# Performance work log

Hardware: AMD Instinct MI355X
Metric: run time of the kernel (lower is better)

## Reference

```python
import jax, jax.numpy as jnp
import numpy as np

B, C, H, W = 4, 64, 128, 128
HID = 256
Q = H * W


def setup_inputs() -> dict:
    key = jax.random.key(0)
    ks = jax.random.split(key, 8)
    inp = jax.random.normal(ks[0], (B, C, H, W), jnp.float32)
    coord = jax.random.uniform(ks[1], (B, Q, 2), jnp.float32, -1.0, 1.0)
    # cell ~ 2/H (size of a high-res pixel in normalized coords), slightly jittered
    cell = (2.0 / H) * (1.0 + 0.1 * jax.random.uniform(ks[2], (B, Q, 2), jnp.float32))
    sc = 1.0 / np.sqrt(C * 9)
    coef_w = jax.random.normal(ks[3], (HID, C, 3, 3), jnp.float32) * sc
    coef_b = jax.random.normal(ks[4], (HID,), jnp.float32) * 0.01
    freq_w = jax.random.normal(ks[5], (HID, C, 3, 3), jnp.float32) * sc
    freq_b = jax.random.normal(ks[6], (HID,), jnp.float32) * 0.01
    phase_w = jax.random.normal(ks[7], (HID // 2, 2), jnp.float32) * 0.5
    return dict(inp=inp, coord=coord, cell=cell, coef_w=coef_w, coef_b=coef_b,
                freq_w=freq_w, freq_b=freq_b, phase_w=phase_w)


def _conv3(x, w, b):
    # 3x3 conv, stride 1, pad 1, NCHW
    y = jax.lax.conv_general_dilated(x, w, (1, 1), ((1, 1), (1, 1)),
                                     dimension_numbers=('NCHW', 'OIHW', 'NCHW'))
    return y + b[None, :, None, None]


def reference(inp, coord, cell, coef_w, coef_b, freq_w, freq_b, phase_w):
    bs, q = coord.shape[0], coord.shape[1]
    h, w = inp.shape[2], inp.shape[3]
    coef = _conv3(inp, coef_w, coef_b)           # (B,HID,H,W)
    freq = _conv3(inp, freq_w, freq_b)           # (B,HID,H,W)
    coef_f = coef.reshape(bs, -1, h * w)
    freq_f = freq.reshape(bs, -1, h * w)
    rx = 1.0 / h                                 # 2/h/2
    ry = 1.0 / w
    eps_shift = 1e-6
    hw = jnp.array([h, w], jnp.float32)
    rel_cell = cell * hw                         # (B,Q,2)
    phase = rel_cell @ phase_w.T                 # (B,Q,HID//2)
    outputs, areas = [], []
    last_raw_area = None
    for vx in (-1.0, 1.0):
        for vy in (-1.0, 1.0):
            c = coord + jnp.array([vx * rx + eps_shift, vy * ry + eps_shift], jnp.float32)
            c = jnp.clip(c, -1.0 + 1e-6, 1.0 - 1e-6)
            # nearest grid_sample, align_corners=False (round-half-even like nearbyint)
            iy = jnp.round(((c[..., 0] + 1.0) * h - 1.0) * 0.5)
            ix = jnp.round(((c[..., 1] + 1.0) * w - 1.0) * 0.5)
            iy = jax.lax.stop_gradient(jnp.clip(iy, 0, h - 1).astype(jnp.int32))
            ix = jax.lax.stop_gradient(jnp.clip(ix, 0, w - 1).astype(jnp.int32))
            idx = iy * w + ix                    # (B,Q)
            q_coef = jnp.take_along_axis(coef_f, idx[:, None, :], axis=2).transpose(0, 2, 1)  # (B,Q,HID)
            q_freq = jnp.take_along_axis(freq_f, idx[:, None, :], axis=2).transpose(0, 2, 1)
            # make_coord value at the gathered pixel
            q_coord = jnp.stack([-1.0 + (2.0 * iy.astype(jnp.float32) + 1.0) / h,
                                 -1.0 + (2.0 * ix.astype(jnp.float32) + 1.0) / w], axis=-1)
            rel = (coord - q_coord) * hw         # (B,Q,2)
            # split q_freq into consecutive pairs, stack -> (B,Q,2,HID//2)
            f = q_freq.reshape(bs, q, -1, 2).swapaxes(-1, -2)
            f = jnp.sum(f * rel[..., None], axis=-2) + phase     # (B,Q,HID//2)
            f = jnp.concatenate([jnp.cos(jnp.pi * f), jnp.sin(jnp.pi * f)], axis=-1)  # (B,Q,HID)
            out = (q_coef * f).reshape(bs, h, w, -1).transpose(0, 3, 1, 2)  # (B,HID,H,W)
            last_raw_area = jnp.abs(rel[..., 0] * rel[..., 1])
            outputs.append(out)
            areas.append(last_raw_area + 1e-9)
    tot_area = areas[0] + areas[1] + areas[2] + areas[3]
    # Faithful to the source: a SINGLE weight from the last corner's raw area
    # is applied to every corner output (the per-corner area swap is unused).
    weight = (last_raw_area / tot_area).reshape(bs, h, w, 1).transpose(0, 3, 1, 2)
    ret = (outputs[0] + outputs[1] + outputs[2] + outputs[3]) * weight
    return ret
```

## Files before the change

kernel.cpp:

```cpp
#include <hip/hip_runtime.h>

typedef unsigned short u16;
typedef _Float16 f16;

#define CIN   64
#define HH    128
#define WW    128
#define NPIX  16384
#define HID   256
#define MTOT  512
#define KTOT  576
#define NB    4
#define WELEM 294912
#define XROW  130
#define XROWS 16900

#define SHM  ((float)(-0.0078125 + 1e-6))
#define SHP  ((float)( 0.0078125 + 1e-6))
#define CLO  ((float)(-1.0 + 1e-6))
#define CHI  ((float)( 1.0 - 1e-6))
#define PIF  3.14159265358979323846f

#define QSCL  1024.0f
#define QISCL (1.0f / 1024.0f)

using f32x4 = __attribute__((ext_vector_type(4))) float;
using f16x8 = __attribute__((ext_vector_type(8))) _Float16;

typedef __attribute__((address_space(1))) const void gas_void;
typedef __attribute__((address_space(3))) void las_void;
__device__ __forceinline__ void gload16(const void* g, void* l) {
  __builtin_amdgcn_global_load_lds((gas_void*)g, (las_void*)l, 16, 0, 0);
}

__device__ __forceinline__ float ldq(const short* p) { return (float)(*p) * QISCL; }
__device__ __forceinline__ void ldqpair(const short* p, float& a, float& b) {
  int u = *(const int*)p;
  a = (float)((short)(u & 0xFFFF)) * QISCL;
  b = (float)((short)(u >> 16)) * QISCL;
}
__device__ __forceinline__ unsigned packq(float a, float b) {
  float fa = fminf(fmaxf(a * QSCL, -32767.f), 32767.f);
  float fb = fminf(fmaxf(b * QSCL, -32767.f), 32767.f);
  int ia = (int)rintf(fa), ib = (int)rintf(fb);
  return ((unsigned)(unsigned short)(short)ia) | (((unsigned)(unsigned short)(short)ib) << 16);
}
__device__ __forceinline__ void storeq4(short* p, float a, float b, float c, float d) {
  uint2 v; v.x = packq(a, b); v.y = packq(c, d);
  *(uint2*)p = v;
}

__global__ __launch_bounds__(256) void lte_prep_w(
    const float* __restrict__ cw, const float* __restrict__ fw,
    f16* __restrict__ Awp) {
  int id = blockIdx.x * 256 + threadIdx.x;
  if (id >= WELEM) return;
  int e  = id & 7;
  int j  = (id >> 3) & 7;
  int i  = (id >> 6) & 127;
  int t2 = id >> 13;
  int mt = t2 / 9;
  int s  = t2 - mt * 9;
  int ch = ((j ^ (i & 7)) << 3) + e;
  int m  = mt * 128 + i;
  const float* src = (m < HID) ? cw : fw;
  Awp[id] = (f16)src[(m & 255) * KTOT + ch * 9 + s];
}

__global__ __launch_bounds__(256) void lte_prep_x(
    const float* __restrict__ inp, f16* __restrict__ xp) {
  int id = blockIdx.x * 256 + threadIdx.x;
  if (id >= NB * XROWS) return;
  int b  = id / XROWS;
  int rr = id - b * XROWS;
  int yy = rr / XROW;
  int x  = rr - yy * XROW - 1;
  int y  = yy - 1;
  f16* op = xp + (size_t)id * 64;
  if ((unsigned)y < 128u && (unsigned)x < 128u) {
    const float* ip = inp + (size_t)b * CIN * NPIX + y * WW + x;
#pragma unroll
    for (int q = 0; q < 8; ++q) {
      f16x8 v;
#pragma unroll
      for (int k = 0; k < 8; ++k) v[k] = (f16)ip[(q * 8 + k) * NPIX];
      *(f16x8*)(op + q * 8) = v;
    }
  } else {
    f16x8 z = {};
#pragma unroll
    for (int q = 0; q < 8; ++q) *(f16x8*)(op + q * 8) = z;
  }
}

__global__ __launch_bounds__(256) void lte_conv_gemm(
    const f16* __restrict__ xp, const f16* __restrict__ Awp,
    const float* __restrict__ coef_b, const float* __restrict__ freq_b,
    short* __restrict__ YT) {
  __shared__ f16 As[2][128 * 64];
  __shared__ f16 Bs[2][128 * 64];

  const int t  = threadIdx.x;
  const int bx = blockIdx.x;
  const int mt = blockIdx.y;
  const int bb = blockIdx.z;
  const int l  = t & 63;
  const int w  = t >> 6;
  const int wr = w >> 1, wc = w & 1;
  const int lm = l & 15;
  const int lm7 = lm & 7;
  const int kq = l >> 4;
  const int lrow = l >> 3;
  const int lchk = l & 7;
  const int w8 = w * 8;

  f32x4 acc[4][4] = {};

  const f16* Atile = Awp + (size_t)(mt * 9) * 8192;
  const f16* xb = xp + (size_t)bb * XROWS * 64;

  auto stage = [&](int s, f16* Ad, f16* Bd) {
    const int ky = s / 3, kx = s - 3 * (s / 3);
    const f16* asrc = Atile + s * 8192;
    const int grow0 = (bx + ky) * XROW + kx;
#pragma unroll
    for (int i = 0; i < 8; ++i) {
      const int c = w8 + i;
      if (c < 16) {
        gload16(asrc + c * 512 + l * 8, Ad + c * 512);
      } else {
        const int cb = c - 16;
        gload16(xb + (size_t)(grow0 + cb * 8 + lrow) * 64 + ((lchk ^ lrow) << 3),
                Bd + cb * 512);
      }
    }
  };

  stage(0, As[0], Bs[0]);
  asm volatile("s_waitcnt vmcnt(0)" ::: "memory");
  __builtin_amdgcn_s_barrier();
  __builtin_amdgcn_sched_barrier(0);

  for (int s = 0; s < 9; ++s) {
    const int cur = s & 1;
    if (s < 8) stage(s + 1, As[cur ^ 1], Bs[cur ^ 1]);
    const f16* Ac = As[cur];
    const f16* Bc = Bs[cur];
#pragma unroll
    for (int ks = 0; ks < 2; ++ks) {
      const int jl = ks * 4 + kq;
      const int pc = (jl ^ lm7) << 3;
      f16x8 af[4], bg[4];
#pragma unroll
      for (int mi = 0; mi < 4; ++mi)
        af[mi] = *(const f16x8*)&Ac[(wr * 64 + mi * 16 + lm) * 64 + pc];
#pragma unroll
      for (int ni = 0; ni < 4; ++ni)
        bg[ni] = *(const f16x8*)&Bc[(wc * 64 + ni * 16 + lm) * 64 + pc];
#pragma unroll
      for (int mi = 0; mi < 4; ++mi)
#pragma unroll
        for (int ni = 0; ni < 4; ++ni)
          acc[mi][ni] = __builtin_amdgcn_mfma_f32_16x16x32_f16(af[mi], bg[ni], acc[mi][ni], 0, 0, 0);
    }
    if (s < 8) {
      asm volatile("s_waitcnt vmcnt(0)" ::: "memory");
      __builtin_amdgcn_s_barrier();
      __builtin_amdgcn_sched_barrier(0);
    }
  }

  const float* bias = (mt < 2) ? (coef_b + mt * 128) : (freq_b + (mt - 2) * 128);
  const int rj = (l >> 4) * 4;
#pragma unroll
  for (int mi = 0; mi < 4; ++mi) {
    const int bm = wr * 64 + mi * 16 + rj;
    const float b0 = bias[bm], b1 = bias[bm + 1], b2 = bias[bm + 2], b3 = bias[bm + 3];
#pragma unroll
    for (int ni = 0; ni < 4; ++ni) {
      const int p = bx * 128 + wc * 64 + ni * 16 + lm;
      size_t off = ((size_t)(bb * NPIX + p)) * 512 + mt * 128 + bm;
      f32x4 v = acc[mi][ni];
      storeq4(&YT[off], v[0] + b0, v[1] + b1, v[2] + b2, v[3] + b3);
    }
  }
}

__global__ __launch_bounds__(128) void lte_sample(
    const short* __restrict__ YT, const float* __restrict__ coord,
    const float* __restrict__ cell, const float* __restrict__ phase_w,
    float* __restrict__ out) {
  __shared__ float lout[256 * 17];
  const int j     = threadIdx.x;
  const int q0    = blockIdx.x * 16;
  const int b     = q0 >> 14;
  const int q0loc = q0 & (NPIX - 1);
  const float pw0 = phase_w[2 * j], pw1 = phase_w[2 * j + 1];
  const short* Yb = YT + ((size_t)b * NPIX) * 512;

  for (int qi = 0; qi < 16; ++qi) {
    const int qg = q0 + qi;
    const float c0  = coord[2 * qg], c1 = coord[2 * qg + 1];
    const float ce0 = cell[2 * qg],  ce1 = cell[2 * qg + 1];
    const float ph  = (ce0 * 128.0f) * pw0 + (ce1 * 128.0f) * pw1;
    float accC = 0.f, accS = 0.f, tot = 0.f, a3 = 0.f;
#pragma unroll
    for (int ci = 0; ci < 4; ++ci) {
      const float s0 = (ci & 2) ? SHP : SHM;
      const float s1 = (ci & 1) ? SHP : SHM;
      float cx = fminf(fmaxf(c0 + s0, CLO), CHI);
      float cy = fminf(fmaxf(c1 + s1, CLO), CHI);
      float ty = ((cx + 1.0f) * 128.0f - 1.0f) * 0.5f;
      float tx = ((cy + 1.0f) * 128.0f - 1.0f) * 0.5f;
      float fy = fminf(fmaxf(rintf(ty), 0.f), 127.f);
      float fx = fminf(fmaxf(rintf(tx), 0.f), 127.f);
      int iy = (int)fy, ix = (int)fx;
      float qcy = -1.0f + (2.0f * fy + 1.0f) * (1.0f / 128.0f);
      float qcx = -1.0f + (2.0f * fx + 1.0f) * (1.0f / 128.0f);
      float rel0 = (c0 - qcy) * 128.0f;
      float rel1 = (c1 - qcx) * 128.0f;
      float ar = fabsf(rel0 * rel1);
      tot += ar + 1e-9f;
      if (ci == 3) a3 = ar;
      const short* bp = Yb + ((size_t)(iy * 128 + ix)) * 512;
      float coefA = ldq(bp + j);
      float coefB = ldq(bp + 128 + j);
      float f0, f1;
      ldqpair(bp + 256 + 2 * j, f0, f1);
      float f = f0 * rel0 + f1 * rel1 + ph;
      float ang = PIF * f;
      accC += coefA * __cosf(ang);
      accS += coefB * __sinf(ang);
    }
    const float wgt = a3 / tot;
    lout[j * 17 + qi]         = accC * wgt;
    lout[(j + 128) * 17 + qi] = accS * wgt;
  }
  __syncthreads();
#pragma unroll
  for (int pass = 0; pass < 8; ++pass) {
    int c  = pass * 32 + (j >> 2);
    int qf = (j & 3) * 4;
    float4 v;
    v.x = lout[c * 17 + qf];     v.y = lout[c * 17 + qf + 1];
    v.z = lout[c * 17 + qf + 2]; v.w = lout[c * 17 + qf + 3];
    *(float4*)(out + (((size_t)(b * 256 + c)) << 14) + q0loc + qf) = v;
  }
}

extern "C" void kernel_launch(void* const* d_in, const int* in_sizes, int n_in,
                              void* d_out, int out_size, void* d_ws, size_t ws_size,
                              hipStream_t stream) {
  const float* inp     = (const float*)d_in[0];
  const float* coord   = (const float*)d_in[1];
  const float* cell    = (const float*)d_in[2];
  const float* coef_w  = (const float*)d_in[3];
  const float* coef_b  = (const float*)d_in[4];
  const float* freq_w  = (const float*)d_in[5];
  const float* freq_b  = (const float*)d_in[6];
  const float* phase_w = (const float*)d_in[7];
  float* out = (float*)d_out;

  f16* Awp = (f16*)d_ws;
  f16* xp  = (f16*)((char*)d_ws + (size_t)WELEM * 2);
  short* YT = (short*)((char*)d_ws + (size_t)WELEM * 2 + (size_t)NB * XROWS * 64 * 2);

  lte_prep_w<<<dim3(1152), dim3(256), 0, stream>>>(coef_w, freq_w, Awp);
  lte_prep_x<<<dim3((NB * XROWS + 255) / 256), dim3(256), 0, stream>>>(inp, xp);
  lte_conv_gemm<<<dim3(128, 4, 4), dim3(256), 0, stream>>>(xp, Awp, coef_b, freq_b, YT);
  lte_sample<<<dim3(4096), dim3(128), 0, stream>>>(YT, coord, cell, phase_w, out);
}
```

Baseline: 126.1 us.

## Load input halo once per conv block and enlarge GEMM tile to 256x256

The conv GEMM block now covers 256 output channels by two image rows (256 pixels) with 512 threads. It loads a 4x136-pixel halo of the padded input into shared memory once, instead of reloading shifted input tiles for each of the nine 3x3 taps. Only the weight tiles stay double-buffered per tap. The input prep kernel now pre-swizzles channel chunks per column so the shifted shared-memory reads stay conflict-free. The trade-off is a larger shared-memory footprint, more accumulators per thread and fewer blocks. The workspace offset also grows, presumably to cover halo reads past the end of the input.

Measured after the change: 129.9 us. 1.03x slower.

```diff
diff --git a/kernel.cpp b/kernel.cpp
--- a/kernel.cpp
+++ b/kernel.cpp
@@ -57,14 +57,13 @@
   if (id >= WELEM) return;
   int e  = id & 7;
   int j  = (id >> 3) & 7;
-  int i  = (id >> 6) & 127;
-  int t2 = id >> 13;
+  int i  = (id >> 6) & 255;
+  int t2 = id >> 14;
   int mt = t2 / 9;
   int s  = t2 - mt * 9;
   int ch = ((j ^ (i & 7)) << 3) + e;
-  int m  = mt * 128 + i;
-  const float* src = (m < HID) ? cw : fw;
-  Awp[id] = (f16)src[(m & 255) * KTOT + ch * 9 + s];
+  const float* src = (mt == 0) ? cw : fw;
+  Awp[id] = (f16)src[i * KTOT + ch * 9 + s];
 }
 
 __global__ __launch_bounds__(256) void lte_prep_x(
@@ -74,16 +73,18 @@
   int b  = id / XROWS;
   int rr = id - b * XROWS;
   int yy = rr / XROW;
-  int x  = rr - yy * XROW - 1;
+  int pc = rr - yy * XROW;
+  int x  = pc - 1;
   int y  = yy - 1;
   f16* op = xp + (size_t)id * 64;
   if ((unsigned)y < 128u && (unsigned)x < 128u) {
     const float* ip = inp + (size_t)b * CIN * NPIX + y * WW + x;
+    const int p7 = pc & 7;
 #pragma unroll
     for (int q = 0; q < 8; ++q) {
       f16x8 v;
 #pragma unroll
-      for (int k = 0; k < 8; ++k) v[k] = (f16)ip[(q * 8 + k) * NPIX];
+      for (int k = 0; k < 8; ++k) v[k] = (f16)ip[(((q ^ p7) << 3) + k) * NPIX];
       *(f16x8*)(op + q * 8) = v;
     }
   } else {
@@ -93,12 +94,12 @@
   }
 }
 
-__global__ __launch_bounds__(256) void lte_conv_gemm(
+__global__ __launch_bounds__(512, 2) void lte_conv_gemm(
     const f16* __restrict__ xp, const f16* __restrict__ Awp,
     const float* __restrict__ coef_b, const float* __restrict__ freq_b,
     short* __restrict__ YT) {
-  __shared__ f16 As[2][128 * 64];
-  __shared__ f16 Bs[2][128 * 64];
+  __shared__ f16 As[2][256 * 64];
+  __shared__ f16 Bs[4 * 136 * 64];
 
   const int t  = threadIdx.x;
   const int bx = blockIdx.x;
@@ -106,61 +107,67 @@
   const int bb = blockIdx.z;
   const int l  = t & 63;
   const int w  = t >> 6;
-  const int wr = w >> 1, wc = w & 1;
+  const int wr = w >> 1;
+  const int wc = w & 1;
   const int lm = l & 15;
   const int lm7 = lm & 7;
   const int kq = l >> 4;
-  const int lrow = l >> 3;
-  const int lchk = l & 7;
-  const int w8 = w * 8;
-
-  f32x4 acc[4][4] = {};
-
-  const f16* Atile = Awp + (size_t)(mt * 9) * 8192;
+  const int w4 = w * 4;
+
+  f32x4 acc[4][8] = {};
+
+  const f16* Atile = Awp + (size_t)(mt * 9) * 16384;
   const f16* xb = xp + (size_t)bb * XROWS * 64;
 
-  auto stage = [&](int s, f16* Ad, f16* Bd) {
-    const int ky = s / 3, kx = s - 3 * (s / 3);
-    const f16* asrc = Atile + s * 8192;
-    const int grow0 = (bx + ky) * XROW + kx;
-#pragma unroll
-    for (int i = 0; i < 8; ++i) {
-      const int c = w8 + i;
-      if (c < 16) {
-        gload16(asrc + c * 512 + l * 8, Ad + c * 512);
-      } else {
-        const int cb = c - 16;
-        gload16(xb + (size_t)(grow0 + cb * 8 + lrow) * 64 + ((lchk ^ lrow) << 3),
-                Bd + cb * 512);
-      }
-    }
-  };
-
-  stage(0, As[0], Bs[0]);
+  {
+    const int yp0 = 2 * bx;
+    for (int c = w; c < 68; c += 8) {
+      const int rr = c / 17, cc = c - rr * 17;
+      gload16(xb + (size_t)((yp0 + rr) * XROW + cc * 8) * 64 + l * 8,
+              Bs + (rr * 136 + cc * 8) * 64);
+    }
+#pragma unroll
+    for (int i = 0; i < 4; ++i) {
+      const int c = w4 + i;
+      gload16(Atile + c * 512 + l * 8, As[0] + c * 512);
+    }
+  }
   asm volatile("s_waitcnt vmcnt(0)" ::: "memory");
   __builtin_amdgcn_s_barrier();
   __builtin_amdgcn_sched_barrier(0);
 
   for (int s = 0; s < 9; ++s) {
     const int cur = s & 1;
-    if (s < 8) stage(s + 1, As[cur ^ 1], Bs[cur ^ 1]);
+    if (s < 8) {
+      const f16* asrc = Atile + (s + 1) * 16384;
+      f16* Ad = As[cur ^ 1];
+#pragma unroll
+      for (int i = 0; i < 4; ++i) {
+        const int c = w4 + i;
+        gload16(asrc + c * 512 + l * 8, Ad + c * 512);
+      }
+    }
+    const int ky = s / 3, kx = s - 3 * (s / 3);
     const f16* Ac = As[cur];
-    const f16* Bc = Bs[cur];
 #pragma unroll
     for (int ks = 0; ks < 2; ++ks) {
       const int jl = ks * 4 + kq;
-      const int pc = (jl ^ lm7) << 3;
-      f16x8 af[4], bg[4];
+      const int pa = (jl ^ lm7) << 3;
+      f16x8 af[4], bg[8];
 #pragma unroll
       for (int mi = 0; mi < 4; ++mi)
-        af[mi] = *(const f16x8*)&Ac[(wr * 64 + mi * 16 + lm) * 64 + pc];
-#pragma unroll
-      for (int ni = 0; ni < 4; ++ni)
-        bg[ni] = *(const f16x8*)&Bc[(wc * 64 + ni * 16 + lm) * 64 + pc];
+        af[mi] = *(const f16x8*)&Ac[(wr * 64 + mi * 16 + lm) * 64 + pa];
+#pragma unroll
+      for (int ni = 0; ni < 8; ++ni) {
+        const int n  = wc * 128 + ni * 16 + lm;
+        const int rr = (n >> 7) + ky;
+        const int xc = (n & 127) + kx;
+        bg[ni] = *(const f16x8*)&Bs[(rr * 136 + xc) * 64 + ((jl ^ (xc & 7)) << 3)];
+      }
 #pragma unroll
       for (int mi = 0; mi < 4; ++mi)
 #pragma unroll
-        for (int ni = 0; ni < 4; ++ni)
+        for (int ni = 0; ni < 8; ++ni)
           acc[mi][ni] = __builtin_amdgcn_mfma_f32_16x16x32_f16(af[mi], bg[ni], acc[mi][ni], 0, 0, 0);
     }
     if (s < 8) {
@@ -170,16 +177,17 @@
     }
   }
 
-  const float* bias = (mt < 2) ? (coef_b + mt * 128) : (freq_b + (mt - 2) * 128);
-  const int rj = (l >> 4) * 4;
+  const float* bias = (mt == 0) ? coef_b : freq_b;
+  const int rj = kq * 4;
 #pragma unroll
   for (int mi = 0; mi < 4; ++mi) {
     const int bm = wr * 64 + mi * 16 + rj;
     const float b0 = bias[bm], b1 = bias[bm + 1], b2 = bias[bm + 2], b3 = bias[bm + 3];
 #pragma unroll
-    for (int ni = 0; ni < 4; ++ni) {
-      const int p = bx * 128 + wc * 64 + ni * 16 + lm;
-      size_t off = ((size_t)(bb * NPIX + p)) * 512 + mt * 128 + bm;
+    for (int ni = 0; ni < 8; ++ni) {
+      const int n = wc * 128 + ni * 16 + lm;
+      const int p = bx * 256 + n;
+      size_t off = ((size_t)(bb * NPIX + p)) * 512 + mt * 256 + bm;
       f32x4 v = acc[mi][ni];
       storeq4(&YT[off], v[0] + b0, v[1] + b1, v[2] + b2, v[3] + b3);
     }
@@ -263,10 +271,11 @@
 
   f16* Awp = (f16*)d_ws;
   f16* xp  = (f16*)((char*)d_ws + (size_t)WELEM * 2);
-  short* YT = (short*)((char*)d_ws + (size_t)WELEM * 2 + (size_t)NB * XROWS * 64 * 2);
+  short* YT = (short*)((char*)d_ws + (size_t)WELEM * 2
+                       + ((size_t)NB * XROWS + 8) * 64 * 2);
 
   lte_prep_w<<<dim3(1152), dim3(256), 0, stream>>>(coef_w, freq_w, Awp);
   lte_prep_x<<<dim3((NB * XROWS + 255) / 256), dim3(256), 0, stream>>>(inp, xp);
-  lte_conv_gemm<<<dim3(128, 4, 4), dim3(256), 0, stream>>>(xp, Awp, coef_b, freq_b, YT);
+  lte_conv_gemm<<<dim3(64, 2, 4), dim3(512), 0, stream>>>(xp, Awp, coef_b, freq_b, YT);
   lte_sample<<<dim3(4096), dim3(128), 0, stream>>>(YT, coord, cell, phase_w, out);
 }
```

## Stage 3-row input halo once in LDS and stream pre-swizzled weights from global

Applied to the files above, without the earlier changes.

The conv GEMM no longer double-buffers A and B tiles for each of the nine filter taps. It now loads a 3-row by 136-column halo of the input into LDS once and reuses it for all taps by shifting the column index. Weight fragments are pre-laid out by the prep kernel in MFMA register order and read straight from global memory, and the input prep applies the XOR swizzle at write time. This removes the per-tap barriers and LDS traffic for A and raises occupancy with launch_bounds(256,3), at the cost of more global and L2 reads for weights and a small workspace offset change for the halo overrun.

After: 132.6 us. 5.1% more time.

```diff
diff --git a/kernel.cpp b/kernel.cpp
--- a/kernel.cpp
+++ b/kernel.cpp
@@ -56,13 +56,17 @@
   int id = blockIdx.x * 256 + threadIdx.x;
   if (id >= WELEM) return;
   int e  = id & 7;
-  int j  = (id >> 3) & 7;
-  int i  = (id >> 6) & 127;
-  int t2 = id >> 13;
-  int mt = t2 / 9;
-  int s  = t2 - mt * 9;
-  int ch = ((j ^ (i & 7)) << 3) + e;
-  int m  = mt * 128 + i;
+  int l  = (id >> 3) & 63;
+  int mi = (id >> 9) & 3;
+  int r  = id >> 11;
+  int ks = r & 1;
+  int r2 = r >> 1;
+  int s  = r2 % 9;
+  int q  = r2 / 9;
+  int wr = q & 1;
+  int mt = q >> 1;
+  int m  = mt * 128 + wr * 64 + mi * 16 + (l & 15);
+  int ch = (ks * 4 + (l >> 4)) * 8 + e;
   const float* src = (m < HID) ? cw : fw;
   Awp[id] = (f16)src[(m & 255) * KTOT + ch * 9 + s];
 }
@@ -74,16 +78,18 @@
   int b  = id / XROWS;
   int rr = id - b * XROWS;
   int yy = rr / XROW;
-  int x  = rr - yy * XROW - 1;
+  int pc = rr - yy * XROW;
+  int x  = pc - 1;
   int y  = yy - 1;
   f16* op = xp + (size_t)id * 64;
   if ((unsigned)y < 128u && (unsigned)x < 128u) {
     const float* ip = inp + (size_t)b * CIN * NPIX + y * WW + x;
+    const int p7 = pc & 7;
 #pragma unroll
     for (int q = 0; q < 8; ++q) {
       f16x8 v;
 #pragma unroll
-      for (int k = 0; k < 8; ++k) v[k] = (f16)ip[(q * 8 + k) * NPIX];
+      for (int k = 0; k < 8; ++k) v[k] = (f16)ip[(((q ^ p7) << 3) + k) * NPIX];
       *(f16x8*)(op + q * 8) = v;
     }
   } else {
@@ -93,12 +99,11 @@
   }
 }
 
-__global__ __launch_bounds__(256) void lte_conv_gemm(
+__global__ __launch_bounds__(256, 3) void lte_conv_gemm(
     const f16* __restrict__ xp, const f16* __restrict__ Awp,
     const float* __restrict__ coef_b, const float* __restrict__ freq_b,
     short* __restrict__ YT) {
-  __shared__ f16 As[2][128 * 64];
-  __shared__ f16 Bs[2][128 * 64];
+  __shared__ f16 Bs[3 * 136 * 64];
 
   const int t  = threadIdx.x;
   const int bx = blockIdx.x;
@@ -106,67 +111,43 @@
   const int bb = blockIdx.z;
   const int l  = t & 63;
   const int w  = t >> 6;
-  const int wr = w >> 1, wc = w & 1;
+  const int wr = __builtin_amdgcn_readfirstlane(w >> 1);
+  const int wc = __builtin_amdgcn_readfirstlane(w & 1);
   const int lm = l & 15;
-  const int lm7 = lm & 7;
-  const int kq = l >> 4;
-  const int lrow = l >> 3;
-  const int lchk = l & 7;
-  const int w8 = w * 8;
 
   f32x4 acc[4][4] = {};
 
-  const f16* Atile = Awp + (size_t)(mt * 9) * 8192;
   const f16* xb = xp + (size_t)bb * XROWS * 64;
-
-  auto stage = [&](int s, f16* Ad, f16* Bd) {
-    const int ky = s / 3, kx = s - 3 * (s / 3);
-    const f16* asrc = Atile + s * 8192;
-    const int grow0 = (bx + ky) * XROW + kx;
-#pragma unroll
-    for (int i = 0; i < 8; ++i) {
-      const int c = w8 + i;
-      if (c < 16) {
-        gload16(asrc + c * 512 + l * 8, Ad + c * 512);
-      } else {
-        const int cb = c - 16;
-        gload16(xb + (size_t)(grow0 + cb * 8 + lrow) * 64 + ((lchk ^ lrow) << 3),
-                Bd + cb * 512);
-      }
-    }
-  };
-
-  stage(0, As[0], Bs[0]);
+  const f16* Aw = Awp + (size_t)((mt * 2 + wr) * 9) * 4096;
+
+  for (int c = w; c < 51; c += 4) {
+    const int rr = c / 17, cc = c - rr * 17;
+    gload16(xb + (size_t)((bx + rr) * XROW + cc * 8) * 64 + l * 8,
+            Bs + (rr * 136 + cc * 8) * 64);
+  }
   asm volatile("s_waitcnt vmcnt(0)" ::: "memory");
   __builtin_amdgcn_s_barrier();
-  __builtin_amdgcn_sched_barrier(0);
 
   for (int s = 0; s < 9; ++s) {
-    const int cur = s & 1;
-    if (s < 8) stage(s + 1, As[cur ^ 1], Bs[cur ^ 1]);
-    const f16* Ac = As[cur];
-    const f16* Bc = Bs[cur];
+    const int ky = s / 3, kx = s - 3 * (s / 3);
+    const f16* As = Aw + s * 4096;
 #pragma unroll
     for (int ks = 0; ks < 2; ++ks) {
-      const int jl = ks * 4 + kq;
-      const int pc = (jl ^ lm7) << 3;
       f16x8 af[4], bg[4];
 #pragma unroll
       for (int mi = 0; mi < 4; ++mi)
-        af[mi] = *(const f16x8*)&Ac[(wr * 64 + mi * 16 + lm) * 64 + pc];
-#pragma unroll
-      for (int ni = 0; ni < 4; ++ni)
-        bg[ni] = *(const f16x8*)&Bc[(wc * 64 + ni * 16 + lm) * 64 + pc];
+        af[mi] = *(const f16x8*)(As + (ks * 4 + mi) * 512 + l * 8);
+      const int jl = ks * 4 + (l >> 4);
+#pragma unroll
+      for (int ni = 0; ni < 4; ++ni) {
+        const int xc = wc * 64 + ni * 16 + lm + kx;
+        bg[ni] = *(const f16x8*)&Bs[(ky * 136 + xc) * 64 + ((jl ^ (xc & 7)) << 3)];
+      }
 #pragma unroll
       for (int mi = 0; mi < 4; ++mi)
 #pragma unroll
         for (int ni = 0; ni < 4; ++ni)
           acc[mi][ni] = __builtin_amdgcn_mfma_f32_16x16x32_f16(af[mi], bg[ni], acc[mi][ni], 0, 0, 0);
-    }
-    if (s < 8) {
-      asm volatile("s_waitcnt vmcnt(0)" ::: "memory");
-      __builtin_amdgcn_s_barrier();
-      __builtin_amdgcn_sched_barrier(0);
     }
   }
 
@@ -263,7 +244,8 @@
 
   f16* Awp = (f16*)d_ws;
   f16* xp  = (f16*)((char*)d_ws + (size_t)WELEM * 2);
-  short* YT = (short*)((char*)d_ws + (size_t)WELEM * 2 + (size_t)NB * XROWS * 64 * 2);
+  short* YT = (short*)((char*)d_ws + (size_t)WELEM * 2
+                       + ((size_t)NB * XROWS + 8) * 64 * 2);
 
   lte_prep_w<<<dim3(1152), dim3(256), 0, stream>>>(coef_w, freq_w, Awp);
   lte_prep_x<<<dim3((NB * XROWS + 255) / 256), dim3(256), 0, stream>>>(inp, xp);
```
